# Optimization experiments

Hardware: AMD Instinct MI355X
Metric: run time of the kernel (lower is better)

The kernel has to match this reference:

```python
import jax, jax.numpy as jnp
import numpy as np
from jax import lax


def setup_inputs() -> dict:
    key = jax.random.key(0)
    ks = jax.random.split(key, 9)
    B, L, d_model = 1, 2048, 1024
    d_inner, d_state, d_conv = 2048, 16, 4

    def g(k, shape, scale):
        return jax.random.normal(k, shape, dtype=jnp.float32) * scale

    return dict(
        x=g(ks[0], (B, L, d_model), 1.0),
        in_proj_w=g(ks[1], (2 * d_inner, d_model), 0.02),   # torch Linear layout (out, in)
        conv_w=g(ks[2], (d_inner, 1, d_conv), 0.1),          # depthwise conv kernel
        conv_b=g(ks[3], (d_inner,), 0.02),
        x_proj_w=g(ks[4], (2 * d_state, d_inner), 0.02),
        dt_proj_w=g(ks[5], (d_inner, d_inner), 0.02),
        dt_proj_b=g(ks[6], (d_inner,), 0.02),
        out_proj_w=g(ks[7], (d_model, d_inner), 0.02),
        A_log=jnp.log(jnp.arange(1, d_state + 1, dtype=jnp.float32)),
        D_param=jnp.ones((d_inner,), dtype=jnp.float32),
    )


def reference(x, in_proj_w, conv_w, conv_b, x_proj_w, dt_proj_w, dt_proj_b,
              out_proj_w, A_log, D_param):
    # x: (B, L, d_model)
    B, L, _ = x.shape
    d_inner = D_param.shape[0]
    d_conv = conv_w.shape[-1]

    xz = x @ in_proj_w.T                       # (B, L, 2*d_inner)
    x_p, z = jnp.split(xz, 2, axis=-1)         # each (B, L, d_inner)

    # causal depthwise conv1d: torch pads d_conv-1 both sides then slices [:L],
    # which equals left-pad d_conv-1 with a valid conv.
    xc = jnp.transpose(x_p, (0, 2, 1))         # (B, d_inner, L)
    xc = lax.conv_general_dilated(
        xc, conv_w, window_strides=(1,), padding=[(d_conv - 1, 0)],
        dimension_numbers=('NCH', 'OIH', 'NCH'), feature_group_count=d_inner)
    xc = xc + conv_b[None, :, None]
    xc = jax.nn.silu(jnp.transpose(xc, (0, 2, 1)))  # (B, L, d_inner)

    # ---- ssm(), mode='tustin'. Note: A_discrete in the original is dead code
    # in tustin mode (never used downstream), so it is omitted.
    dt = jax.nn.softplus(xc @ dt_proj_w.T + dt_proj_b)   # (B, L, d_inner)
    BC = xc @ x_proj_w.T                                 # (B, L, 2*d_state)
    B_ssm, C_ssm = jnp.split(BC, 2, axis=-1)             # (B, L, d_state) each

    # Original: B_disc = dt[...,None] * B_ssm[:, :, None, :]  (B,L,D,N)
    #           y = einsum('bld,bldn->bln', xc, B_disc)
    # This contraction factorizes: sum_d xc*dt is independent of n.
    s = jnp.sum(xc * dt, axis=-1, keepdims=True)          # (B, L, 1)
    y = s * B_ssm                                         # (B, L, d_state)
    y = y * C_ssm                                         # einsum('bln,n->bln', ., ones) * C
    # Original does y.sum(-1) + xc * D; keepdims makes the broadcast well-defined.
    y = jnp.sum(y, axis=-1, keepdims=True) + xc * D_param  # (B, L, d_inner)

    y = y * jax.nn.silu(z)
    return y @ out_proj_w.T                                # (B, L, d_model)
```

## Files before the change

kernel.cpp:

```cpp
#include <hip/hip_runtime.h>
#include <hip/hip_bf16.h>

typedef __attribute__((ext_vector_type(8))) short bf16x8;
typedef __attribute__((ext_vector_type(4))) float f32x4;

__device__ __forceinline__ float b2f(unsigned short u) {
  union { float f; unsigned int i; } v; v.i = ((unsigned int)u) << 16; return v.f;
}
__device__ __forceinline__ unsigned short f2b(float f) {
  __hip_bfloat16 h = __float2bfloat16(f);
  union { __hip_bfloat16 h; unsigned short u; } v; v.h = h; return v.u;
}

#define F32_MAGIC 0x3F800000u

#define GLDS16(g, l)                                                        \
  __builtin_amdgcn_global_load_lds(                                         \
      (const __attribute__((address_space(1))) void*)(g),                   \
      (__attribute__((address_space(3))) void*)(l), 16, 0, 0)

__global__ __launch_bounds__(256) void cast4_k(const void* __restrict__ s0, unsigned short* __restrict__ d0,
                                               const void* __restrict__ s1, unsigned short* __restrict__ d1,
                                               const void* __restrict__ s2, unsigned short* __restrict__ d2,
                                               const void* __restrict__ s3, unsigned short* __restrict__ d3,
                                               const unsigned int* __restrict__ dpw) {
  const int i = blockIdx.x * 256 + threadIdx.x;
  const void* s; unsigned short* d; int off;
  if      (i <  262144) { s = s0; d = d0; off = i; }
  else if (i <  786432) { s = s1; d = d1; off = i - 262144; }
  else if (i < 1310720) { s = s2; d = d2; off = i - 786432; }
  else if (i < 1572864) { s = s3; d = d3; off = i - 1310720; }
  else return;
  const bool src_f32 = (dpw[0] == F32_MAGIC);
  bf16x8 o;
  if (src_f32) {
    const float* p = (const float*)s + (size_t)off * 8;
#pragma unroll
    for (int j = 0; j < 8; ++j) o[j] = (short)f2b(p[j]);
  } else {
    o = *(const bf16x8*)((const unsigned short*)s + (size_t)off * 8);
  }
  *(bf16x8*)(d + (size_t)off * 8) = o;
}

__global__ __launch_bounds__(256) void cast_small_k(const void* __restrict__ s0, unsigned short* __restrict__ d0,
                                                    const void* __restrict__ s1, unsigned short* __restrict__ d1,
                                                    const void* __restrict__ s2, unsigned short* __restrict__ d2,
                                                    const void* __restrict__ s3, unsigned short* __restrict__ d3,
                                                    const void* __restrict__ s4, unsigned short* __restrict__ d4,
                                                    const unsigned int* __restrict__ dpw) {
  const int i = blockIdx.x * 256 + threadIdx.x;
  const void* s; unsigned short* d; int off;
  if      (i < 8192) { s = s0; d = d0; off = i; }
  else if (i < 9216) { s = s1; d = d1; off = i - 8192; }
  else if (i < 9472) { s = s2; d = d2; off = i - 9216; }
  else if (i < 9728) { s = s3; d = d3; off = i - 9472; }
  else if (i < 9984) { s = s4; d = d4; off = i - 9728; }
  else return;
  const bool src_f32 = (dpw[0] == F32_MAGIC);
  bf16x8 o;
  if (src_f32) {
    const float* p = (const float*)s + (size_t)off * 8;
#pragma unroll
    for (int j = 0; j < 8; ++j) o[j] = (short)f2b(p[j]);
  } else {
    o = *(const bf16x8*)((const unsigned short*)s + (size_t)off * 8);
  }
  *(bf16x8*)(d + (size_t)off * 8) = o;
}

template <int BM, int BN, int BK, int DEPTH, int MODE>
__global__ __launch_bounds__(256) void gemm_nt(const unsigned short* __restrict__ A,
                                               const unsigned short* __restrict__ B,
                                               void* __restrict__ C,
                                               int M, int N, int K,
                                               const unsigned short* __restrict__ bias,
                                               const unsigned int* __restrict__ dpw) {
  constexpr int CPR = BK / 8;
  constexpr int CPRL = (BK == 64) ? 3 : 2;
  constexpr int LPS_A = BM * BK / 2048;
  constexpr int LPS_B = BN * BK / 2048;
  constexpr int LPS = LPS_A + LPS_B;
  constexpr int WM = BM / 2, WN = BN / 2;
  constexpr int MI = WM / 16, NJ = WN / 16;
  constexpr int KK = BK / 32;

  __shared__ unsigned short As[DEPTH][BM * BK];
  __shared__ unsigned short Bs[DEPTH][BN * BK];

  const int tid = threadIdx.x;
  const int lane = tid & 63;
  const int wave = tid >> 6;
  const int m0 = blockIdx.x * BM;
  const int n0 = blockIdx.y * BN;
  const int wm = (wave >> 1) * WM;
  const int wn = (wave & 1) * WN;
  const int lr = lane & 15;
  const int lu = lane >> 4;

  f32x4 acc[MI][NJ];
#pragma unroll
  for (int i = 0; i < MI; ++i)
#pragma unroll
    for (int j = 0; j < NJ; ++j) acc[i][j] = (f32x4){0.f, 0.f, 0.f, 0.f};

  const int nk = K / BK;

  auto stage = [&](int t, int buf) {
    const int k0 = t * BK;
#pragma unroll
    for (int p = 0; p < LPS_A; ++p) {
      const int c = tid + p * 256;
      const int row = c >> CPRL;
      const int scol = ((c & (CPR - 1)) ^ (row & (CPR - 1))) * 8;
      GLDS16(A + (size_t)(m0 + row) * K + k0 + scol, &As[buf][c * 8]);
    }
#pragma unroll
    for (int p = 0; p < LPS_B; ++p) {
      const int c = tid + p * 256;
      const int row = c >> CPRL;
      const int scol = ((c & (CPR - 1)) ^ (row & (CPR - 1))) * 8;
      GLDS16(B + (size_t)(n0 + row) * K + k0 + scol, &Bs[buf][c * 8]);
    }
  };

#pragma unroll
  for (int i = 0; i < DEPTH - 1; ++i)
    if (i < nk) stage(i, i);

  int cur = 0;
  for (int t = 0; t < nk; ++t) {
    const int ahead = nk - 1 - t;
    if (ahead >= DEPTH - 2) {
      asm volatile("s_waitcnt vmcnt(%0)" ::"n"((DEPTH - 2) * LPS) : "memory");
    } else if (ahead == 2) {
      asm volatile("s_waitcnt vmcnt(%0)" ::"n"(2 * LPS) : "memory");
    } else if (ahead == 1) {
      asm volatile("s_waitcnt vmcnt(%0)" ::"n"(LPS) : "memory");
    } else {
      asm volatile("s_waitcnt vmcnt(0)" ::: "memory");
    }
    __builtin_amdgcn_s_barrier();

    const int ts = t + DEPTH - 1;
    const int sbuf = (cur == 0) ? DEPTH - 1 : cur - 1;
    if (ts < nk) stage(ts, sbuf);

#pragma unroll
    for (int kk = 0; kk < KK; ++kk) {
      bf16x8 af[MI], bfr[NJ];
#pragma unroll
      for (int i = 0; i < MI; ++i) {
        const int row = wm + i * 16 + lr;
        const int unit = (kk * 4 + lu) ^ (row & (CPR - 1));
        af[i] = *(const bf16x8*)(&As[cur][row * BK + unit * 8]);
      }
#pragma unroll
      for (int j = 0; j < NJ; ++j) {
        const int row = wn + j * 16 + lr;
        const int unit = (kk * 4 + lu) ^ (row & (CPR - 1));
        bfr[j] = *(const bf16x8*)(&Bs[cur][row * BK + unit * 8]);
      }
#pragma unroll
      for (int i = 0; i < MI; ++i)
#pragma unroll
        for (int j = 0; j < NJ; ++j)
          acc[i][j] = __builtin_amdgcn_mfma_f32_16x16x32_bf16(af[i], bfr[j], acc[i][j], 0, 0, 0);
    }
    cur = (cur + 1 == DEPTH) ? 0 : cur + 1;
  }

  const int cr = lu * 4;
  const int cc = lane & 15;
  const bool f32out = (MODE == 2) ? (dpw[0] == F32_MAGIC) : false;
#pragma unroll
  for (int i = 0; i < MI; ++i)
#pragma unroll
    for (int j = 0; j < NJ; ++j) {
      const int n = n0 + wn + j * 16 + cc;
#pragma unroll
      for (int r = 0; r < 4; ++r) {
        const size_t off = (size_t)(m0 + wm + i * 16 + cr + r) * N + n;
        float v = acc[i][j][r];
        if (MODE == 0) {
          ((unsigned short*)C)[off] = f2b(v);
        } else if (MODE == 1) {
          float pre = v + b2f(bias[n]);
          float dt = (pre > 20.f) ? pre : log1pf(expf(pre));
          ((unsigned short*)C)[off] = f2b(dt);
        } else {
          if (f32out) ((float*)C)[off] = v;
          else        ((unsigned short*)C)[off] = f2b(v);
        }
      }
    }
}

__global__ __launch_bounds__(256) void gemm_bc_k(const unsigned short* __restrict__ A,
                                                 const unsigned short* __restrict__ B,
                                                 float* __restrict__ C, int K, int Nfull) {
  __shared__ float red[4][16][16];
  const int m0 = blockIdx.x * 16;
  const int n0 = blockIdx.y * 16;
  const int tid = threadIdx.x;
  const int wave = tid >> 6;
  const int lane = tid & 63;
  const int lr = lane & 15;
  const int lk = (lane >> 4) * 8;
  const int kslice = K / 4;

  f32x4 acc = (f32x4){0.f, 0.f, 0.f, 0.f};
  const int kbeg = wave * kslice;
  for (int k0 = kbeg; k0 < kbeg + kslice; k0 += 32) {
    bf16x8 a = *(const bf16x8*)(A + (size_t)(m0 + lr) * K + k0 + lk);
    bf16x8 b = *(const bf16x8*)(B + (size_t)(n0 + lr) * K + k0 + lk);
    acc = __builtin_amdgcn_mfma_f32_16x16x32_bf16(a, b, acc, 0, 0, 0);
  }
  const int cr = (lane >> 4) * 4;
#pragma unroll
  for (int r = 0; r < 4; ++r) red[wave][cr + r][lr] = acc[r];
  __syncthreads();
  if (wave == 0) {
#pragma unroll
    for (int r = 0; r < 4; ++r) {
      float s = red[0][cr + r][lr] + red[1][cr + r][lr] + red[2][cr + r][lr] + red[3][cr + r][lr];
      C[(size_t)(m0 + cr + r) * Nfull + n0 + lr] = s;
    }
  }
}

__global__ __launch_bounds__(256) void conv_silu_k(const unsigned short* __restrict__ xz,
                                                   const unsigned short* __restrict__ cw,
                                                   const unsigned short* __restrict__ cb,
                                                   unsigned short* __restrict__ xc) {
  const int idx = blockIdx.x * 256 + threadIdx.x;
  const int l = idx >> 8;
  const int d0 = (idx & 255) * 8;

  float acc[8];
  bf16x8 bias = *(const bf16x8*)(cb + d0);
#pragma unroll
  for (int j = 0; j < 8; ++j) acc[j] = b2f((unsigned short)bias[j]);

  float wv[32];
#pragma unroll
  for (int q = 0; q < 4; ++q) {
    bf16x8 v = *(const bf16x8*)(cw + (size_t)d0 * 4 + q * 8);
#pragma unroll
    for (int e = 0; e < 8; ++e) wv[q * 8 + e] = b2f((unsigned short)v[e]);
  }

#pragma unroll
  for (int t = 0; t < 4; ++t) {
    const int row = l - 3 + t;
    if (row >= 0) {
      bf16x8 v = *(const bf16x8*)(xz + (size_t)row * 4096 + d0);
#pragma unroll
      for (int j = 0; j < 8; ++j) acc[j] += b2f((unsigned short)v[j]) * wv[j * 4 + t];
    }
  }

  bf16x8 o;
#pragma unroll
  for (int j = 0; j < 8; ++j) {
    float s = acc[j];
    s = s / (1.f + expf(-s));
    o[j] = (short)f2b(s);
  }
  *(bf16x8*)(xc + (size_t)l * 2048 + d0) = o;
}

__global__ __launch_bounds__(256) void combine_k(const unsigned short* __restrict__ dt16,
                                                 const float* __restrict__ BC,
                                                 unsigned short* __restrict__ xc,
                                                 const unsigned short* __restrict__ xz,
                                                 const unsigned short* __restrict__ Dp) {
  const int l = blockIdx.x;
  const int t = threadIdx.x;
  const int d0 = t * 8;

  bf16x8 xcv = *(const bf16x8*)(xc + (size_t)l * 2048 + d0);
  bf16x8 dtv = *(const bf16x8*)(dt16 + (size_t)l * 2048 + d0);

  float xf[8];
  float s = 0.f;
#pragma unroll
  for (int j = 0; j < 8; ++j) {
    xf[j] = b2f((unsigned short)xcv[j]);
    s += xf[j] * b2f((unsigned short)dtv[j]);
  }

#pragma unroll
  for (int off = 32; off > 0; off >>= 1) s += __shfl_down(s, off, 64);

  __shared__ float red[4];
  __shared__ float sb;
  const int lane = t & 63, wv = t >> 6;
  if (lane == 0) red[wv] = s;
  __syncthreads();
  if (t == 0) {
    float ss = red[0] + red[1] + red[2] + red[3];
    float bc = 0.f;
    const float* bcp = BC + (size_t)l * 32;
#pragma unroll
    for (int n = 0; n < 16; ++n) bc += bcp[n] * bcp[16 + n];
    sb = ss * bc;
  }
  __syncthreads();
  const float ypre = sb;

  bf16x8 zv = *(const bf16x8*)(xz + (size_t)l * 4096 + 2048 + d0);
  bf16x8 dv = *(const bf16x8*)(Dp + d0);
  bf16x8 o;
#pragma unroll
  for (int j = 0; j < 8; ++j) {
    float z = b2f((unsigned short)zv[j]);
    float yv = (ypre + xf[j] * b2f((unsigned short)dv[j])) * (z / (1.f + expf(-z)));
    o[j] = (short)f2b(yv);
  }
  *(bf16x8*)(xc + (size_t)l * 2048 + d0) = o;
}

extern "C" void kernel_launch(void* const* d_in, const int* in_sizes, int n_in,
                              void* d_out, int out_size, void* d_ws, size_t ws_size,
                              hipStream_t stream) {
  const void* x_raw   = d_in[0];
  const void* wi_raw  = d_in[1];
  const void* cw_raw  = d_in[2];
  const void* cb_raw  = d_in[3];
  const void* xw_raw  = d_in[4];
  const void* dtw_raw = d_in[5];
  const void* dtb_raw = d_in[6];
  const void* ow_raw  = d_in[7];
  const void* dp_raw  = d_in[9];
  const unsigned int* dpw = (const unsigned int*)dp_raw;

  char* ws = (char*)d_ws;
  const size_t MB = 1u << 20;
  unsigned short* xb   = (unsigned short*)(ws + 0 * MB);
  unsigned short* wib  = (unsigned short*)(ws + 4 * MB);
  unsigned short* dtwb = (unsigned short*)(ws + 12 * MB);
  unsigned short* owb  = (unsigned short*)(ws + 20 * MB);
  unsigned short* xwb  = (unsigned short*)(ws + 24 * MB);
  unsigned short* cwb  = (unsigned short*)(ws + 24 * MB + 256 * 1024);
  unsigned short* cbb  = (unsigned short*)(ws + 24 * MB + 320 * 1024);
  unsigned short* dtbb = (unsigned short*)(ws + 24 * MB + 384 * 1024);
  unsigned short* dpb  = (unsigned short*)(ws + 24 * MB + 448 * 1024);
  unsigned short* xz   = (unsigned short*)(ws + 25 * MB);
  unsigned short* xc   = (unsigned short*)(ws + 41 * MB);
  float*          BC   = (float*)(ws + 0 * MB);
  unsigned short* dt16 = (unsigned short*)(ws + 4 * MB);

  const int L = 2048, DM = 1024, DI = 2048;

  cast4_k<<<6144, 256, 0, stream>>>(x_raw, xb, wi_raw, wib, dtw_raw, dtwb, ow_raw, owb, dpw);
  cast_small_k<<<39, 256, 0, stream>>>(xw_raw, xwb, cw_raw, cwb, cb_raw, cbb,
                                       dtb_raw, dtbb, dp_raw, dpb, dpw);

  gemm_nt<128, 128, 32, 5, 0><<<dim3(16, 32), 256, 0, stream>>>(xb, wib, xz, L, 2 * DI, DM, nullptr, dpw);
  conv_silu_k<<<dim3(2048), 256, 0, stream>>>(xz, cwb, cbb, xc);
  gemm_nt<128, 64, 64, 3, 1><<<dim3(16, 32), 256, 0, stream>>>(xc, dtwb, dt16, L, DI, DI, dtbb, dpw);
  gemm_bc_k<<<dim3(128, 2), 256, 0, stream>>>(xc, xwb, BC, DI, 32);
  combine_k<<<dim3(2048), 256, 0, stream>>>(dt16, BC, xc, xz, dpb);
  gemm_nt<64, 64, 64, 3, 2><<<dim3(32, 16), 256, 0, stream>>>(xc, owb, d_out, L, DM, DI, nullptr, dpw);
}
```

Measured before the change: 139.3 us.

## Fuse fp32 weight-to-bf16 conversion into GEMM loads, dropping separate weight cast

The separate cast pass over the three large weight matrices is removed. Each GEMM now reads fp32 weights straight into registers, converts them to bf16 and writes them to LDS, while activations still use direct global-to-LDS loads. The pipeline is rebuilt as a fixed triple-buffered A / double-buffered B scheme with an extra XOR swizzle. This saves one full read and write of the weights, but the weights now always read as fp32 (twice the bytes, re-read by every tile), and the old dtype check on the weights is gone.

```diff
diff --git a/kernel.cpp b/kernel.cpp
--- a/kernel.cpp
+++ b/kernel.cpp
@@ -19,28 +19,21 @@
       (const __attribute__((address_space(1))) void*)(g),                   \
       (__attribute__((address_space(3))) void*)(l), 16, 0, 0)
 
-__global__ __launch_bounds__(256) void cast4_k(const void* __restrict__ s0, unsigned short* __restrict__ d0,
-                                               const void* __restrict__ s1, unsigned short* __restrict__ d1,
-                                               const void* __restrict__ s2, unsigned short* __restrict__ d2,
-                                               const void* __restrict__ s3, unsigned short* __restrict__ d3,
-                                               const unsigned int* __restrict__ dpw) {
+__global__ __launch_bounds__(256) void cast_x_k(const void* __restrict__ src,
+                                                unsigned short* __restrict__ dst,
+                                                int n8, const unsigned int* __restrict__ dpw) {
   const int i = blockIdx.x * 256 + threadIdx.x;
-  const void* s; unsigned short* d; int off;
-  if      (i <  262144) { s = s0; d = d0; off = i; }
-  else if (i <  786432) { s = s1; d = d1; off = i - 262144; }
-  else if (i < 1310720) { s = s2; d = d2; off = i - 786432; }
-  else if (i < 1572864) { s = s3; d = d3; off = i - 1310720; }
-  else return;
+  if (i >= n8) return;
   const bool src_f32 = (dpw[0] == F32_MAGIC);
   bf16x8 o;
   if (src_f32) {
-    const float* p = (const float*)s + (size_t)off * 8;
+    const float* p = (const float*)src + (size_t)i * 8;
 #pragma unroll
     for (int j = 0; j < 8; ++j) o[j] = (short)f2b(p[j]);
   } else {
-    o = *(const bf16x8*)((const unsigned short*)s + (size_t)off * 8);
-  }
-  *(bf16x8*)(d + (size_t)off * 8) = o;
+    o = *(const bf16x8*)((const unsigned short*)src + (size_t)i * 8);
+  }
+  *(bf16x8*)(dst + (size_t)i * 8) = o;
 }
 
 __global__ __launch_bounds__(256) void cast_small_k(const void* __restrict__ s0, unsigned short* __restrict__ d0,
@@ -69,9 +62,9 @@
   *(bf16x8*)(d + (size_t)off * 8) = o;
 }
 
-template <int BM, int BN, int BK, int DEPTH, int MODE>
+template <int BM, int BN, int BK, int MODE>
 __global__ __launch_bounds__(256) void gemm_nt(const unsigned short* __restrict__ A,
-                                               const unsigned short* __restrict__ B,
+                                               const float* __restrict__ Bf,
                                                void* __restrict__ C,
                                                int M, int N, int K,
                                                const unsigned short* __restrict__ bias,
@@ -80,13 +73,15 @@
   constexpr int CPRL = (BK == 64) ? 3 : 2;
   constexpr int LPS_A = BM * BK / 2048;
   constexpr int LPS_B = BN * BK / 2048;
-  constexpr int LPS = LPS_A + LPS_B;
+  constexpr int ASTEP = BM * BK * 2;
+  constexpr int BSTEP = BN * BK * 2;
   constexpr int WM = BM / 2, WN = BN / 2;
   constexpr int MI = WM / 16, NJ = WN / 16;
   constexpr int KK = BK / 32;
-
-  __shared__ unsigned short As[DEPTH][BM * BK];
-  __shared__ unsigned short Bs[DEPTH][BN * BK];
+  constexpr int NENTRY = LPS_A;
+  constexpr int NPRO = 2 * LPS_A + 2 * LPS_B;
+
+  __shared__ char lds[3 * ASTEP + 2 * BSTEP];
 
   const int tid = threadIdx.x;
   const int lane = tid & 63;
@@ -98,77 +93,140 @@
   const int lr = lane & 15;
   const int lu = lane >> 4;
 
+  auto swz = [](int u, int row) {
+    int s = u ^ (row & (CPR - 1));
+    if (CPR == 4) s ^= (row >> 2) & 3;
+    return s & (CPR - 1);
+  };
+
   f32x4 acc[MI][NJ];
 #pragma unroll
   for (int i = 0; i < MI; ++i)
 #pragma unroll
     for (int j = 0; j < NJ; ++j) acc[i][j] = (f32x4){0.f, 0.f, 0.f, 0.f};
 
+  const unsigned short* aG[LPS_A];
+  const float* bG[LPS_B];
+  int aL[LPS_A];
+  int bW[LPS_B];
+#pragma unroll
+  for (int p = 0; p < LPS_A; ++p) {
+    const int c = tid + p * 256;
+    const int row = c >> CPRL, u = c & (CPR - 1);
+    aG[p] = A + (size_t)(m0 + row) * K + swz(u, row) * 8;
+    aL[p] = c * 16;
+  }
+#pragma unroll
+  for (int q = 0; q < LPS_B; ++q) {
+    const int c = tid + q * 256;
+    const int row = c >> CPRL, u = c & (CPR - 1);
+    bG[q] = Bf + (size_t)(n0 + row) * K + u * 8;
+    bW[q] = (row * BK + swz(u, row) * 8) * 2;
+  }
+  int aR[MI][KK], bR[NJ][KK];
+#pragma unroll
+  for (int i = 0; i < MI; ++i)
+#pragma unroll
+    for (int kk = 0; kk < KK; ++kk) {
+      const int row = wm + i * 16 + lr;
+      aR[i][kk] = (row * BK + swz(kk * 4 + lu, row) * 8) * 2;
+    }
+#pragma unroll
+  for (int j = 0; j < NJ; ++j)
+#pragma unroll
+    for (int kk = 0; kk < KK; ++kk) {
+      const int row = wn + j * 16 + lr;
+      bR[j][kk] = (row * BK + swz(kk * 4 + lu, row) * 8) * 2;
+    }
+
+  f32x4 rB0[LPS_B][2], rB1[LPS_B][2];
+
+#define STAGE_B(REGS)                                            \
+  do {                                                           \
+    _Pragma("unroll") for (int q = 0; q < LPS_B; ++q) {          \
+      REGS[q][0] = *(const f32x4*)(bG[q]);                       \
+      REGS[q][1] = *(const f32x4*)(bG[q] + 4);                   \
+      bG[q] += BK;                                               \
+    }                                                            \
+  } while (0)
+
+#define STAGE_A(abytes)                                          \
+  do {                                                           \
+    _Pragma("unroll") for (int p = 0; p < LPS_A; ++p) {          \
+      GLDS16(aG[p], lds + (abytes) + aL[p]);                     \
+      aG[p] += BK;                                               \
+    }                                                            \
+  } while (0)
+
+#define WRITE_B(REGS, bbytes)                                    \
+  do {                                                           \
+    _Pragma("unroll") for (int q = 0; q < LPS_B; ++q) {          \
+      bf16x8 o;                                                  \
+      _Pragma("unroll") for (int e = 0; e < 4; ++e) {            \
+        o[e] = (short)f2b(REGS[q][0][e]);                        \
+        o[e + 4] = (short)f2b(REGS[q][1][e]);                    \
+      }                                                          \
+      *(bf16x8*)(lds + 3 * ASTEP + (bbytes) + bW[q]) = o;        \
+    }                                                            \
+  } while (0)
+
+#define COMPUTE(abytes, bbytes)                                                  \
+  do {                                                                          \
+    _Pragma("unroll") for (int kk = 0; kk < KK; ++kk) {                         \
+      bf16x8 af[MI], bfr[NJ];                                                   \
+      _Pragma("unroll") for (int i = 0; i < MI; ++i)                            \
+          af[i] = *(const bf16x8*)(lds + (abytes) + aR[i][kk]);                 \
+      _Pragma("unroll") for (int j = 0; j < NJ; ++j)                            \
+          bfr[j] = *(const bf16x8*)(lds + 3 * ASTEP + (bbytes) + bR[j][kk]);    \
+      _Pragma("unroll") for (int i = 0; i < MI; ++i)                            \
+          _Pragma("unroll") for (int j = 0; j < NJ; ++j)                        \
+              acc[i][j] =                                                       \
+          __builtin_amdgcn_mfma_f32_16x16x32_bf16(af[i], bfr[j], acc[i][j], 0, 0, 0); \
+    }                                                                           \
+  } while (0)
+
   const int nk = K / BK;
 
-  auto stage = [&](int t, int buf) {
-    const int k0 = t * BK;
-#pragma unroll
-    for (int p = 0; p < LPS_A; ++p) {
-      const int c = tid + p * 256;
-      const int row = c >> CPRL;
-      const int scol = ((c & (CPR - 1)) ^ (row & (CPR - 1))) * 8;
-      GLDS16(A + (size_t)(m0 + row) * K + k0 + scol, &As[buf][c * 8]);
-    }
-#pragma unroll
-    for (int p = 0; p < LPS_B; ++p) {
-      const int c = tid + p * 256;
-      const int row = c >> CPRL;
-      const int scol = ((c & (CPR - 1)) ^ (row & (CPR - 1))) * 8;
-      GLDS16(B + (size_t)(n0 + row) * K + k0 + scol, &Bs[buf][c * 8]);
-    }
-  };
-
-#pragma unroll
-  for (int i = 0; i < DEPTH - 1; ++i)
-    if (i < nk) stage(i, i);
-
-  int cur = 0;
-  for (int t = 0; t < nk; ++t) {
-    const int ahead = nk - 1 - t;
-    if (ahead >= DEPTH - 2) {
-      asm volatile("s_waitcnt vmcnt(%0)" ::"n"((DEPTH - 2) * LPS) : "memory");
-    } else if (ahead == 2) {
-      asm volatile("s_waitcnt vmcnt(%0)" ::"n"(2 * LPS) : "memory");
-    } else if (ahead == 1) {
-      asm volatile("s_waitcnt vmcnt(%0)" ::"n"(LPS) : "memory");
-    } else {
-      asm volatile("s_waitcnt vmcnt(0)" ::: "memory");
-    }
-    __builtin_amdgcn_s_barrier();
-
-    const int ts = t + DEPTH - 1;
-    const int sbuf = (cur == 0) ? DEPTH - 1 : cur - 1;
-    if (ts < nk) stage(ts, sbuf);
-
-#pragma unroll
-    for (int kk = 0; kk < KK; ++kk) {
-      bf16x8 af[MI], bfr[NJ];
-#pragma unroll
-      for (int i = 0; i < MI; ++i) {
-        const int row = wm + i * 16 + lr;
-        const int unit = (kk * 4 + lu) ^ (row & (CPR - 1));
-        af[i] = *(const bf16x8*)(&As[cur][row * BK + unit * 8]);
-      }
-#pragma unroll
-      for (int j = 0; j < NJ; ++j) {
-        const int row = wn + j * 16 + lr;
-        const int unit = (kk * 4 + lu) ^ (row & (CPR - 1));
-        bfr[j] = *(const bf16x8*)(&Bs[cur][row * BK + unit * 8]);
-      }
-#pragma unroll
-      for (int i = 0; i < MI; ++i)
-#pragma unroll
-        for (int j = 0; j < NJ; ++j)
-          acc[i][j] = __builtin_amdgcn_mfma_f32_16x16x32_bf16(af[i], bfr[j], acc[i][j], 0, 0, 0);
-    }
-    cur = (cur + 1 == DEPTH) ? 0 : cur + 1;
-  }
+  STAGE_B(rB0);
+  STAGE_A(0);
+  STAGE_B(rB1);
+  STAGE_A(ASTEP);
+  asm volatile("s_waitcnt vmcnt(%0)" ::"n"(NPRO) : "memory");
+  WRITE_B(rB0, 0);
+
+  int acb = 0;
+  int asb = 2 * ASTEP;
+  int bcb = 0;
+
+#define ITER(t, LDs, WRs)                                                   \
+  do {                                                                      \
+    if ((t) < nk - 1) {                                                     \
+      asm volatile("s_waitcnt vmcnt(%0) lgkmcnt(0)" ::"n"(NENTRY) : "memory"); \
+    } else {                                                                \
+      asm volatile("s_waitcnt vmcnt(0) lgkmcnt(0)" ::: "memory");           \
+    }                                                                       \
+    __builtin_amdgcn_s_barrier();                                           \
+    if ((t) + 1 < nk) WRITE_B(WRs, bcb ^ BSTEP);                            \
+    if ((t) + 2 < nk) {                                                     \
+      STAGE_B(LDs);                                                         \
+      STAGE_A(asb);                                                         \
+    }                                                                       \
+    COMPUTE(acb, bcb);                                                      \
+    acb = (acb == 2 * ASTEP) ? 0 : acb + ASTEP;                             \
+    asb = (asb == 2 * ASTEP) ? 0 : asb + ASTEP;                             \
+    bcb ^= BSTEP;                                                           \
+  } while (0)
+
+  for (int t = 0; t < nk; t += 2) {
+    ITER(t, rB0, rB1);
+    ITER(t + 1, rB1, rB0);
+  }
+
+#undef ITER
+#undef COMPUTE
+#undef WRITE_B
+#undef STAGE_A
+#undef STAGE_B
 
   const int cr = lu * 4;
   const int cc = lane & 15;
@@ -325,42 +383,39 @@
                               void* d_out, int out_size, void* d_ws, size_t ws_size,
                               hipStream_t stream) {
   const void* x_raw   = d_in[0];
-  const void* wi_raw  = d_in[1];
+  const float* wi_f   = (const float*)d_in[1];
   const void* cw_raw  = d_in[2];
   const void* cb_raw  = d_in[3];
   const void* xw_raw  = d_in[4];
-  const void* dtw_raw = d_in[5];
+  const float* dtw_f  = (const float*)d_in[5];
   const void* dtb_raw = d_in[6];
-  const void* ow_raw  = d_in[7];
+  const float* ow_f   = (const float*)d_in[7];
   const void* dp_raw  = d_in[9];
   const unsigned int* dpw = (const unsigned int*)dp_raw;
 
   char* ws = (char*)d_ws;
   const size_t MB = 1u << 20;
   unsigned short* xb   = (unsigned short*)(ws + 0 * MB);
-  unsigned short* wib  = (unsigned short*)(ws + 4 * MB);
-  unsigned short* dtwb = (unsigned short*)(ws + 12 * MB);
-  unsigned short* owb  = (unsigned short*)(ws + 20 * MB);
-  unsigned short* xwb  = (unsigned short*)(ws + 24 * MB);
-  unsigned short* cwb  = (unsigned short*)(ws + 24 * MB + 256 * 1024);
-  unsigned short* cbb  = (unsigned short*)(ws + 24 * MB + 320 * 1024);
-  unsigned short* dtbb = (unsigned short*)(ws + 24 * MB + 384 * 1024);
-  unsigned short* dpb  = (unsigned short*)(ws + 24 * MB + 448 * 1024);
-  unsigned short* xz   = (unsigned short*)(ws + 25 * MB);
-  unsigned short* xc   = (unsigned short*)(ws + 41 * MB);
-  float*          BC   = (float*)(ws + 0 * MB);
-  unsigned short* dt16 = (unsigned short*)(ws + 4 * MB);
+  unsigned short* xwb  = (unsigned short*)(ws + 4 * MB);
+  unsigned short* cwb  = (unsigned short*)(ws + 4 * MB + 256 * 1024);
+  unsigned short* cbb  = (unsigned short*)(ws + 4 * MB + 320 * 1024);
+  unsigned short* dtbb = (unsigned short*)(ws + 4 * MB + 384 * 1024);
+  unsigned short* dpb  = (unsigned short*)(ws + 4 * MB + 448 * 1024);
+  unsigned short* xz   = (unsigned short*)(ws + 5 * MB);
+  unsigned short* xc   = (unsigned short*)(ws + 21 * MB);
+  unsigned short* dt16 = (unsigned short*)(ws + 29 * MB);
+  float*          BC   = (float*)(ws + 37 * MB);
 
   const int L = 2048, DM = 1024, DI = 2048;
 
-  cast4_k<<<6144, 256, 0, stream>>>(x_raw, xb, wi_raw, wib, dtw_raw, dtwb, ow_raw, owb, dpw);
+  cast_x_k<<<1024, 256, 0, stream>>>(x_raw, xb, (L * DM) / 8, dpw);
   cast_small_k<<<39, 256, 0, stream>>>(xw_raw, xwb, cw_raw, cwb, cb_raw, cbb,
                                        dtb_raw, dtbb, dp_raw, dpb, dpw);
 
-  gemm_nt<128, 128, 32, 5, 0><<<dim3(16, 32), 256, 0, stream>>>(xb, wib, xz, L, 2 * DI, DM, nullptr, dpw);
+  gemm_nt<128, 128, 32, 0><<<dim3(16, 32), 256, 0, stream>>>(xb, wi_f, xz, L, 2 * DI, DM, nullptr, dpw);
   conv_silu_k<<<dim3(2048), 256, 0, stream>>>(xz, cwb, cbb, xc);
-  gemm_nt<128, 64, 64, 3, 1><<<dim3(16, 32), 256, 0, stream>>>(xc, dtwb, dt16, L, DI, DI, dtbb, dpw);
+  gemm_nt<128, 64, 64, 1><<<dim3(16, 32), 256, 0, stream>>>(xc, dtw_f, dt16, L, DI, DI, dtbb, dpw);
   gemm_bc_k<<<dim3(128, 2), 256, 0, stream>>>(xc, xwb, BC, DI, 32);
   combine_k<<<dim3(2048), 256, 0, stream>>>(dt16, BC, xc, xz, dpb);
-  gemm_nt<64, 64, 64, 3, 2><<<dim3(32, 16), 256, 0, stream>>>(xc, owb, d_out, L, DM, DI, nullptr, dpw);
-}
+  gemm_nt<64, 64, 64, 2><<<dim3(32, 16), 256, 0, stream>>>(xc, ow_f, d_out, L, DM, DI, nullptr, dpw);
+}
```

New measurement: 129.0 us. -7.4%, faster.

## Precompute GEMM address offsets, add XOR swizzle, shrink tiles for more blocks

Applied to the files above, without the earlier changes.

The GEMM main loop now works from precomputed global pointers and LDS byte offsets that advance each step, replacing per-iteration index math. For BK=32 it uses a stronger XOR swizzle to cut LDS bank conflicts, and it adds a scheduling fence after the barrier. The in_proj and dt_proj GEMMs switch to smaller tiles, launching more blocks for better CU occupancy. In exchange, each block reuses fewer loaded tiles and more operand data is re-fetched, and keeping the precomputed offsets in registers raises register pressure.

```diff
diff --git a/kernel.cpp b/kernel.cpp
--- a/kernel.cpp
+++ b/kernel.cpp
@@ -18,6 +18,12 @@
   __builtin_amdgcn_global_load_lds(                                         \
       (const __attribute__((address_space(1))) void*)(g),                   \
       (__attribute__((address_space(3))) void*)(l), 16, 0, 0)
+
+#define POST_BARRIER_FENCE()                  \
+  do {                                        \
+    asm volatile("" ::: "memory");            \
+    __builtin_amdgcn_sched_barrier(0);        \
+  } while (0)
 
 __global__ __launch_bounds__(256) void cast4_k(const void* __restrict__ s0, unsigned short* __restrict__ d0,
                                                const void* __restrict__ s1, unsigned short* __restrict__ d1,
@@ -81,12 +87,14 @@
   constexpr int LPS_A = BM * BK / 2048;
   constexpr int LPS_B = BN * BK / 2048;
   constexpr int LPS = LPS_A + LPS_B;
+  constexpr int ASTEP = BM * BK * 2;
+  constexpr int BSTEP = BN * BK * 2;
   constexpr int WM = BM / 2, WN = BN / 2;
   constexpr int MI = WM / 16, NJ = WN / 16;
   constexpr int KK = BK / 32;
 
-  __shared__ unsigned short As[DEPTH][BM * BK];
-  __shared__ unsigned short Bs[DEPTH][BN * BK];
+  __shared__ char lds[DEPTH * (ASTEP + BSTEP)];
+  constexpr int BBASE = DEPTH * ASTEP;
 
   const int tid = threadIdx.x;
   const int lane = tid & 63;
@@ -98,76 +106,107 @@
   const int lr = lane & 15;
   const int lu = lane >> 4;
 
+  auto swz = [](int u, int row) {
+    int s = u ^ (row & (CPR - 1));
+    if (CPR == 4) s ^= (row >> 2) & 3;
+    return s & (CPR - 1);
+  };
+
   f32x4 acc[MI][NJ];
 #pragma unroll
   for (int i = 0; i < MI; ++i)
 #pragma unroll
     for (int j = 0; j < NJ; ++j) acc[i][j] = (f32x4){0.f, 0.f, 0.f, 0.f};
 
+  const unsigned short* aG[LPS_A];
+  const unsigned short* bG[LPS_B];
+  int aL[LPS_A], bL[LPS_B];
+#pragma unroll
+  for (int p = 0; p < LPS_A; ++p) {
+    const int c = tid + p * 256;
+    const int row = c >> CPRL, u = c & (CPR - 1);
+    aG[p] = A + (size_t)(m0 + row) * K + swz(u, row) * 8;
+    aL[p] = c * 16;
+  }
+#pragma unroll
+  for (int q = 0; q < LPS_B; ++q) {
+    const int c = tid + q * 256;
+    const int row = c >> CPRL, u = c & (CPR - 1);
+    bG[q] = B + (size_t)(n0 + row) * K + swz(u, row) * 8;
+    bL[q] = c * 16;
+  }
+  int aR[MI][KK], bR[NJ][KK];
+#pragma unroll
+  for (int i = 0; i < MI; ++i)
+#pragma unroll
+    for (int kk = 0; kk < KK; ++kk) {
+      const int row = wm + i * 16 + lr;
+      aR[i][kk] = (row * BK + swz(kk * 4 + lu, row) * 8) * 2;
+    }
+#pragma unroll
+  for (int j = 0; j < NJ; ++j)
+#pragma unroll
+    for (int kk = 0; kk < KK; ++kk) {
+      const int row = wn + j * 16 + lr;
+      bR[j][kk] = (row * BK + swz(kk * 4 + lu, row) * 8) * 2;
+    }
+
   const int nk = K / BK;
 
-  auto stage = [&](int t, int buf) {
-    const int k0 = t * BK;
+  auto stage = [&](int ab, int bb) {
 #pragma unroll
     for (int p = 0; p < LPS_A; ++p) {
-      const int c = tid + p * 256;
-      const int row = c >> CPRL;
-      const int scol = ((c & (CPR - 1)) ^ (row & (CPR - 1))) * 8;
-      GLDS16(A + (size_t)(m0 + row) * K + k0 + scol, &As[buf][c * 8]);
-    }
-#pragma unroll
-    for (int p = 0; p < LPS_B; ++p) {
-      const int c = tid + p * 256;
-      const int row = c >> CPRL;
-      const int scol = ((c & (CPR - 1)) ^ (row & (CPR - 1))) * 8;
-      GLDS16(B + (size_t)(n0 + row) * K + k0 + scol, &Bs[buf][c * 8]);
+      GLDS16(aG[p], lds + ab + aL[p]);
+      aG[p] += BK;
+    }
+#pragma unroll
+    for (int q = 0; q < LPS_B; ++q) {
+      GLDS16(bG[q], lds + BBASE + bb + bL[q]);
+      bG[q] += BK;
     }
   };
 
 #pragma unroll
   for (int i = 0; i < DEPTH - 1; ++i)
-    if (i < nk) stage(i, i);
-
-  int cur = 0;
+    if (i < nk) stage(i * ASTEP, i * BSTEP);
+
+  int acb = 0, bcb = 0;
+  int asb = (DEPTH - 1) * ASTEP, bsb = (DEPTH - 1) * BSTEP;
+
   for (int t = 0; t < nk; ++t) {
     const int ahead = nk - 1 - t;
-    if (ahead >= DEPTH - 2) {
+    if (DEPTH >= 4 && ahead >= DEPTH - 2) {
       asm volatile("s_waitcnt vmcnt(%0)" ::"n"((DEPTH - 2) * LPS) : "memory");
-    } else if (ahead == 2) {
-      asm volatile("s_waitcnt vmcnt(%0)" ::"n"(2 * LPS) : "memory");
-    } else if (ahead == 1) {
+    } else if (DEPTH >= 3 && ahead >= 1 && (DEPTH < 4 || ahead == 1)) {
       asm volatile("s_waitcnt vmcnt(%0)" ::"n"(LPS) : "memory");
     } else {
       asm volatile("s_waitcnt vmcnt(0)" ::: "memory");
     }
     __builtin_amdgcn_s_barrier();
-
-    const int ts = t + DEPTH - 1;
-    const int sbuf = (cur == 0) ? DEPTH - 1 : cur - 1;
-    if (ts < nk) stage(ts, sbuf);
+    POST_BARRIER_FENCE();
+
+    if (t + DEPTH - 1 < nk) stage(asb, bsb);
 
 #pragma unroll
     for (int kk = 0; kk < KK; ++kk) {
       bf16x8 af[MI], bfr[NJ];
 #pragma unroll
-      for (int i = 0; i < MI; ++i) {
-        const int row = wm + i * 16 + lr;
-        const int unit = (kk * 4 + lu) ^ (row & (CPR - 1));
-        af[i] = *(const bf16x8*)(&As[cur][row * BK + unit * 8]);
-      }
-#pragma unroll
-      for (int j = 0; j < NJ; ++j) {
-        const int row = wn + j * 16 + lr;
-        const int unit = (kk * 4 + lu) ^ (row & (CPR - 1));
-        bfr[j] = *(const bf16x8*)(&Bs[cur][row * BK + unit * 8]);
-      }
+      for (int i = 0; i < MI; ++i)
+        af[i] = *(const bf16x8*)(lds + acb + aR[i][kk]);
+#pragma unroll
+      for (int j = 0; j < NJ; ++j)
+        bfr[j] = *(const bf16x8*)(lds + BBASE + bcb + bR[j][kk]);
 #pragma unroll
       for (int i = 0; i < MI; ++i)
 #pragma unroll
         for (int j = 0; j < NJ; ++j)
           acc[i][j] = __builtin_amdgcn_mfma_f32_16x16x32_bf16(af[i], bfr[j], acc[i][j], 0, 0, 0);
     }
-    cur = (cur + 1 == DEPTH) ? 0 : cur + 1;
+
+    acb = (acb == (DEPTH - 1) * ASTEP) ? 0 : acb + ASTEP;
+    bcb = (bcb == (DEPTH - 1) * BSTEP) ? 0 : bcb + BSTEP;
+    asb = (asb == (DEPTH - 1) * ASTEP) ? 0 : asb + ASTEP;
+    bsb = (bsb == (DEPTH - 1) * BSTEP) ? 0 : bsb + BSTEP;
   }
 
   const int cr = lu * 4;
@@ -357,9 +396,9 @@
   cast_small_k<<<39, 256, 0, stream>>>(xw_raw, xwb, cw_raw, cwb, cb_raw, cbb,
                                        dtb_raw, dtbb, dp_raw, dpb, dpw);
 
-  gemm_nt<128, 128, 32, 5, 0><<<dim3(16, 32), 256, 0, stream>>>(xb, wib, xz, L, 2 * DI, DM, nullptr, dpw);
+  gemm_nt<128, 64, 32, 4, 0><<<dim3(16, 64), 256, 0, stream>>>(xb, wib, xz, L, 2 * DI, DM, nullptr, dpw);
   conv_silu_k<<<dim3(2048), 256, 0, stream>>>(xz, cwb, cbb, xc);
-  gemm_nt<128, 64, 64, 3, 1><<<dim3(16, 32), 256, 0, stream>>>(xc, dtwb, dt16, L, DI, DI, dtbb, dpw);
+  gemm_nt<64, 64, 64, 3, 1><<<dim3(32, 32), 256, 0, stream>>>(xc, dtwb, dt16, L, DI, DI, dtbb, dpw);
   gemm_bc_k<<<dim3(128, 2), 256, 0, stream>>>(xc, xwb, BC, DI, 32);
   combine_k<<<dim3(2048), 256, 0, stream>>>(dt16, BC, xc, xz, dpb);
   gemm_nt<64, 64, 64, 3, 2><<<dim3(32, 16), 256, 0, stream>>>(xc, owb, d_out, L, DM, DI, nullptr, dpw);
```

Measured after the change: 132.9 us. 4.6% less time.
